# Kernel optimization log

Hardware: AMD Instinct MI355X
Metric: run time of the kernel (lower is better)

The kernel has to match this reference:

```python
import jax, jax.numpy as jnp
import numpy as np

NB = 256  # images are quantized to 256 intensity levels (uint8 pipeline)


def _histograms(q):
    # q: int32 (BC, N) values in [0, NB)
    BC, N = q.shape
    idx = (q + jnp.arange(BC, dtype=jnp.int32)[:, None] * NB).reshape(-1)
    ones = jnp.ones((BC * N,), dtype=jnp.int32)
    return jax.ops.segment_sum(ones, idx, num_segments=BC * NB).reshape(BC, NB)


def _match_lut(counts_s, counts_r):
    # Fixed-shape emulation of the per-channel np.unique/cumsum/np.interp loop.
    occ_s = counts_s > 0
    occ_r = counts_r > 0
    first_s = jnp.argmax(occ_s)  # smallest unique source value (dropped, maps to 0)
    first_r = jnp.argmax(occ_r)  # smallest unique reference value (dropped)
    cs = counts_s.at[first_s].set(0)
    cr = counts_r.at[first_r].set(0)
    cums = jnp.cumsum(cs).astype(jnp.float32)
    cumr = jnp.cumsum(cr).astype(jnp.float32)
    s_q = cums / jnp.maximum(cums[-1], 1.0)  # source quantiles at every bin
    r_q = cumr / jnp.maximum(cumr[-1], 1.0)
    # Compact occupied reference bins (excluding the first) to the front so that
    # jnp.interp sees only the quantiles/values that np.unique would produce.
    occ_r2 = occ_r & (jnp.arange(NB) != first_r)
    order = jnp.argsort(jnp.logical_not(occ_r2))  # stable: occupied bins first, ascending
    occ_sorted = occ_r2[order]
    xp = jnp.where(occ_sorted, r_q[order], 2.0)   # pad with x>1 so queries (<=1) never reach pads
    fp = jnp.where(occ_sorted, order.astype(jnp.float32), 0.0)
    lut = jnp.trunc(jnp.interp(s_q, xp, fp))  # trunc == C-style cast into uint8 result buffer
    lut = lut.at[first_s].set(0.0)            # interp_value[0] = 0 in the original
    ok = (jnp.sum(occ_s) > 1) & (jnp.sum(occ_r) > 1)  # 'continue' branch -> zeros
    return jnp.where(ok, lut, 0.0)


def _match_histogram(source, reference):
    # source/reference: float (B,3,H,W) with values at exact 0..255 levels
    B, C, H, W = source.shape
    sq = jnp.clip(jnp.round(source), 0, NB - 1).astype(jnp.int32).reshape(B * C, H * W)
    rq = jnp.clip(jnp.round(reference), 0, NB - 1).astype(jnp.int32).reshape(B * C, H * W)
    lut = jax.vmap(_match_lut)(_histograms(sq), _histograms(rq))  # (BC, NB)
    return jnp.take_along_axis(lut, sq, axis=1).reshape(B, C, H, W)


def reference(input_data, target_data, ref_data, mask_src, mask_tar):
    to_img = lambda x: (x + 1.0) * 0.5 * 255.0  # tensor2image(x) * 255
    inp = to_img(input_data)
    tar = to_img(target_data)
    ref = to_img(ref_data)
    m_src = jnp.broadcast_to(mask_src, inp.shape)
    m_tar = jnp.broadcast_to(mask_tar, tar.shape)
    input_masked = inp * m_src
    target_masked = tar * m_tar
    ref_masked = ref * m_src
    matched = jax.lax.stop_gradient(_match_histogram(ref_masked, target_masked))
    input_match = matched * m_src
    return jnp.mean(jnp.abs(input_masked - input_match))  # L1Loss


def setup_inputs() -> dict:
    key = jax.random.key(0)
    k1, k2, k3, k4, k5 = jax.random.split(key, 5)
    B, H, W = 8, 512, 512

    def img(k):
        # exact multiples of 1/255 in [-1,1] -> integer 0..255 after tensor2image*255
        levels = jax.random.randint(k, (B, 3, H, W), 0, 256).astype(jnp.float32)
        return (levels / 255.0) * 2.0 - 1.0

    def mask(k):
        return (jax.random.uniform(k, (B, 1, H, W)) > 0.3).astype(jnp.float32)

    return {
        "input_data": img(k1),
        "target_data": img(k2),
        "ref_data": img(k3),
        "mask_src": mask(k4),
        "mask_tar": mask(k5),
    }
```

## Files before the change

### kernel.cpp

```cpp
#include <hip/hip_runtime.h>

#define HW    262144
#define HW4   65536
#define BC    24
#define NB    256
#define NTOT  6291456

#define GH    64
#define GL    64
#define TOTL  (BC * GL)

#define WS_HSP_OFF   0
#define WS_HRP_OFF   1572864
#define WS_LUT_OFF   3145728
#define WS_LSUM_OFF  3170304
#define WS_QB_OFF    3176448
#define WS_MB_OFF    9467904

__device__ __forceinline__ int quantize(float x, float m) {
    float v = (x + 1.0f) * 0.5f * 255.0f * m;
    float r = rintf(v);
    r = fminf(fmaxf(r, 0.0f), 255.0f);
    return (int)r;
}

__device__ __forceinline__ int incl_scan256(int v, int t, int* buf4, int* tot) {
    const int lane = t & 63;
    const int wave = t >> 6;
#pragma unroll
    for (int off = 1; off < 64; off <<= 1) {
        int y = __shfl_up(v, off, 64);
        if (lane >= off) v += y;
    }
    __syncthreads();
    if (lane == 63) buf4[wave] = v;
    __syncthreads();
    int add = 0;
#pragma unroll
    for (int w = 0; w < 4; ++w) if (w < wave) add += buf4[w];
    *tot = buf4[0] + buf4[1] + buf4[2] + buf4[3];
    return v + add;
}

__global__ void __launch_bounds__(256)
hist_kernel(const float4* __restrict__ ref4,
            const float4* __restrict__ tar4,
            const float4* __restrict__ ms4,
            const float4* __restrict__ mt4,
            int* __restrict__ hsPart, int* __restrict__ hrPart,
            uchar4* __restrict__ qb, unsigned short* __restrict__ mb) {
    __shared__ int wh[4 * 2 * NB];
    const int t = threadIdx.x;
    const int wave = t >> 6;
    const int lane = t & 63;
#pragma unroll
    for (int j = 0; j < 8; ++j) wh[t + j * 256] = 0;
    __syncthreads();

    const int c = blockIdx.y;
    const int b = c / 3;
    const float4* refc = ref4 + (size_t)c * HW4;
    const float4* tarc = tar4 + (size_t)c * HW4;
    const float4* msb  = ms4 + (size_t)b * HW4;
    const float4* mtb  = mt4 + (size_t)b * HW4;
    uchar4* qbc = qb + (size_t)c * HW4;
    unsigned short* mbc = mb + (size_t)c * (GH * 256);

    const int base = blockIdx.x * 256 + t;

    float4 R[4], T[4], M[4], MT[4];
#pragma unroll
    for (int j = 0; j < 4; ++j) R[j]  = refc[base + j * 16384];
#pragma unroll
    for (int j = 0; j < 4; ++j) M[j]  = msb[base + j * 16384];
#pragma unroll
    for (int j = 0; j < 4; ++j) T[j]  = tarc[base + j * 16384];
#pragma unroll
    for (int j = 0; j < 4; ++j) MT[j] = mtb[base + j * 16384];

    int* whS = &wh[wave * 512];
    int* whR = &wh[wave * 512 + 256];
    int n0s = 0, n0r = 0;
    unsigned mbits = 0u;
#pragma unroll
    for (int j = 0; j < 4; ++j) {
        const float rv[4]  = {R[j].x, R[j].y, R[j].z, R[j].w};
        const float mv[4]  = {M[j].x, M[j].y, M[j].z, M[j].w};
        const float tvv[4] = {T[j].x, T[j].y, T[j].z, T[j].w};
        const float mtv[4] = {MT[j].x, MT[j].y, MT[j].z, MT[j].w};
        unsigned q8[4];
#pragma unroll
        for (int k = 0; k < 4; ++k) {
            const int qs = quantize(rv[k], mv[k]);
            q8[k] = (unsigned)qs;
            if (mv[k] != 0.0f) { atomicAdd(&whS[qs], 1); mbits |= 1u << (j * 4 + k); }
            else n0s++;
            if (mtv[k] != 0.0f) atomicAdd(&whR[quantize(tvv[k], mtv[k])], 1);
            else n0r++;
        }
        uchar4 qq;
        qq.x = (unsigned char)q8[0];
        qq.y = (unsigned char)q8[1];
        qq.z = (unsigned char)q8[2];
        qq.w = (unsigned char)q8[3];
        qbc[base + j * 16384] = qq;
    }
    mbc[base] = (unsigned short)mbits;

#pragma unroll
    for (int off = 32; off > 0; off >>= 1) {
        n0s += __shfl_down(n0s, off);
        n0r += __shfl_down(n0r, off);
    }
    if (lane == 0) {
        if (n0s) atomicAdd(&whS[0], n0s);
        if (n0r) atomicAdd(&whR[0], n0r);
    }
    __syncthreads();

    const int s = wh[t] + wh[512 + t] + wh[1024 + t] + wh[1536 + t];
    const int r = wh[256 + t] + wh[768 + t] + wh[1280 + t] + wh[1792 + t];
    hsPart[(c * GH + blockIdx.x) * NB + t] = s;
    hrPart[(c * GH + blockIdx.x) * NB + t] = r;
}

__global__ void __launch_bounds__(256)
lut_kernel(const int* __restrict__ hsPart,
           const int* __restrict__ hrPart,
           float* __restrict__ lut) {
    const int c = blockIdx.x;
    const int t = threadIdx.x;

    __shared__ int   buf4[4];
    __shared__ float xp[NB];
    __shared__ float fp[NB];
    __shared__ int firstS, firstR, nOccS, nOccR;

    int cs = 0, cr = 0;
#pragma unroll 8
    for (int g = 0; g < GH; ++g) {
        cs += hsPart[(c * GH + g) * NB + t];
        cr += hrPart[(c * GH + g) * NB + t];
    }

    if (t == 0) { firstS = NB; firstR = NB; nOccS = 0; nOccR = 0; }
    __syncthreads();
    if (cs > 0) { atomicMin(&firstS, t); atomicAdd(&nOccS, 1); }
    if (cr > 0) { atomicMin(&firstR, t); atomicAdd(&nOccR, 1); }
    __syncthreads();

    const int csz = (t == firstS) ? 0 : cs;
    const int crz = (t == firstR) ? 0 : cr;

    int totS, totR, dummy;
    const int cumS = incl_scan256(csz, t, buf4, &totS);
    const int cumR = incl_scan256(crz, t, buf4, &totR);
    const int occ2 = (cr > 0 && t != firstR) ? 1 : 0;
    const int rank = incl_scan256(occ2, t, buf4, &dummy) - occ2;

    const float x  = (float)cumS / fmaxf((float)totS, 1.0f);
    const float rq = (float)cumR / fmaxf((float)totR, 1.0f);

    xp[t] = 2.0f;
    fp[t] = 0.0f;
    __syncthreads();
    if (occ2) { xp[rank] = rq; fp[rank] = (float)t; }
    __syncthreads();

    int lo = 0, hi = NB;
    while (lo < hi) {
        int mid = (lo + hi) >> 1;
        if (xp[mid] > x) hi = mid; else lo = mid + 1;
    }
    int i2 = lo;
    i2 = (i2 < 1) ? 1 : ((i2 > NB - 1) ? NB - 1 : i2);
    float dxv = xp[i2] - xp[i2 - 1];
    float f;
    if (dxv == 0.0f) f = fp[i2];
    else f = fp[i2 - 1] + (x - xp[i2 - 1]) / dxv * (fp[i2] - fp[i2 - 1]);
    if (x < xp[0]) f = fp[0];

    float l = truncf(f);
    if (t == firstS) l = 0.0f;
    if (!((nOccS > 1) && (nOccR > 1))) l = 0.0f;

    lut[c * NB + t] = l;
}

__global__ void __launch_bounds__(256)
loss_kernel(const float4* __restrict__ inp4,
            const uchar4* __restrict__ qb,
            const unsigned short* __restrict__ mb,
            const float* __restrict__ lut,
            float* __restrict__ lsum) {
    __shared__ float llut[NB];
    __shared__ float wsum[4];
    const int t = threadIdx.x;
    const int c = blockIdx.y;
    const int g = blockIdx.x;
    const int lane = t & 63;
    const int wave = t >> 6;

    const float4* inpc = inp4 + (size_t)c * HW4;
    const uchar4* qbc  = qb + (size_t)c * HW4;
    const unsigned short* mbc = mb + (size_t)c * (GL * 256);
    const int base = g * 256 + t;

    float4 X[4];
    uchar4 Q[4];
#pragma unroll
    for (int j = 0; j < 4; ++j) X[j] = inpc[base + j * 16384];
#pragma unroll
    for (int j = 0; j < 4; ++j) Q[j] = qbc[base + j * 16384];
    const unsigned mbits = (unsigned)mbc[base];

    llut[t] = lut[c * NB + t];
    __syncthreads();

    float s = 0.0f;
#pragma unroll
    for (int j = 0; j < 4; ++j) {
        const float xv[4] = {X[j].x, X[j].y, X[j].z, X[j].w};
        const unsigned qv[4] = {Q[j].x, Q[j].y, Q[j].z, Q[j].w};
#pragma unroll
        for (int k = 0; k < 4; ++k) {
            const float mf = (float)((mbits >> (j * 4 + k)) & 1u);
            const float im = (xv[k] + 1.0f) * 127.5f;
            s += mf * fabsf(im - llut[qv[k]]);
        }
    }

#pragma unroll
    for (int off = 32; off > 0; off >>= 1) s += __shfl_down(s, off);
    if (lane == 0) wsum[wave] = s;
    __syncthreads();
    if (t == 0)
        lsum[c * GL + g] = wsum[0] + wsum[1] + wsum[2] + wsum[3];
}

__global__ void __launch_bounds__(256)
finalize_kernel(const float* __restrict__ lsum, float* __restrict__ out) {
    const int t = threadIdx.x;
    float s = 0.0f;
#pragma unroll
    for (int i = t; i < TOTL; i += 256) s += lsum[i];
#pragma unroll
    for (int off = 32; off > 0; off >>= 1) s += __shfl_down(s, off);
    __shared__ float wsum[4];
    const int lane = t & 63;
    const int wave = t >> 6;
    if (lane == 0) wsum[wave] = s;
    __syncthreads();
    if (t == 0)
        out[0] = (wsum[0] + wsum[1] + wsum[2] + wsum[3]) / (float)NTOT;
}

extern "C" void kernel_launch(void* const* d_in, const int* in_sizes, int n_in,
                              void* d_out, int out_size, void* d_ws, size_t ws_size,
                              hipStream_t stream) {
    const float* inp  = (const float*)d_in[0];
    const float* tar  = (const float*)d_in[1];
    const float* ref  = (const float*)d_in[2];
    const float* msrc = (const float*)d_in[3];
    const float* mtar = (const float*)d_in[4];

    char* ws = (char*)d_ws;
    int*            hsPart = (int*)(ws + WS_HSP_OFF);
    int*            hrPart = (int*)(ws + WS_HRP_OFF);
    float*          lut    = (float*)(ws + WS_LUT_OFF);
    float*          lsum   = (float*)(ws + WS_LSUM_OFF);
    uchar4*         qb     = (uchar4*)(ws + WS_QB_OFF);
    unsigned short* mb     = (unsigned short*)(ws + WS_MB_OFF);

    hist_kernel<<<dim3(GH, BC), 256, 0, stream>>>(
        (const float4*)ref, (const float4*)tar,
        (const float4*)msrc, (const float4*)mtar,
        hsPart, hrPart, qb, mb);

    lut_kernel<<<BC, 256, 0, stream>>>(hsPart, hrPart, lut);

    loss_kernel<<<dim3(GL, BC), 256, 0, stream>>>(
        (const float4*)inp, qb, mb, lut, lsum);

    finalize_kernel<<<1, 256, 0, stream>>>(lsum, (float*)d_out);
}
```

Measured before the change: 129.0 us.

## Split histogram merge into its own kernel and fuse LUT build into loss

Replaces the 24-block LUT kernel with a merge kernel that sums the partial histograms across 48 blocks, one per channel and histogram. Each loss block then rebuilds the channel LUT itself (scans, binary-search interp) while its input loads are in flight. The intent is to widen parallelism on the serial LUT stage and overlap LUT construction with the loss loads. In exchange, the scan and interp work is repeated in each of the 64 loss blocks per channel, and the loss kernel uses more shared memory and registers.

```diff
diff --git a/kernel.cpp b/kernel.cpp
--- a/kernel.cpp
+++ b/kernel.cpp
@@ -12,10 +12,11 @@
 
 #define WS_HSP_OFF   0
 #define WS_HRP_OFF   1572864
-#define WS_LUT_OFF   3145728
-#define WS_LSUM_OFF  3170304
-#define WS_QB_OFF    3176448
-#define WS_MB_OFF    9467904
+#define WS_HSF_OFF   3145728
+#define WS_HRF_OFF   3170304
+#define WS_LSUM_OFF  3194880
+#define WS_QB_OFF    3201024
+#define WS_MB_OFF    9492480
 
 __device__ __forceinline__ int quantize(float x, float m) {
     float v = (x + 1.0f) * 0.5f * 255.0f * m;
@@ -125,23 +126,53 @@
 }
 
 __global__ void __launch_bounds__(256)
-lut_kernel(const int* __restrict__ hsPart,
-           const int* __restrict__ hrPart,
-           float* __restrict__ lut) {
-    const int c = blockIdx.x;
-    const int t = threadIdx.x;
-
+merge_kernel(const int* __restrict__ hsPart, const int* __restrict__ hrPart,
+             int* __restrict__ histS, int* __restrict__ histR) {
+    const int c = blockIdx.y;
+    const int t = threadIdx.x;
+    const int* __restrict__ src = blockIdx.x ? hrPart : hsPart;
+    int* __restrict__ dst       = blockIdx.x ? histR : histS;
+    int s = 0;
+#pragma unroll 8
+    for (int g = 0; g < GH; ++g) s += src[(c * GH + g) * NB + t];
+    dst[c * NB + t] = s;
+}
+
+__global__ void __launch_bounds__(256)
+loss_kernel(const float4* __restrict__ inp4,
+            const uchar4* __restrict__ qb,
+            const unsigned short* __restrict__ mb,
+            const int* __restrict__ histS,
+            const int* __restrict__ histR,
+            float* __restrict__ lsum) {
     __shared__ int   buf4[4];
     __shared__ float xp[NB];
     __shared__ float fp[NB];
+    __shared__ float llut[NB];
+    __shared__ float wsum[4];
     __shared__ int firstS, firstR, nOccS, nOccR;
 
-    int cs = 0, cr = 0;
-#pragma unroll 8
-    for (int g = 0; g < GH; ++g) {
-        cs += hsPart[(c * GH + g) * NB + t];
-        cr += hrPart[(c * GH + g) * NB + t];
-    }
+    const int t = threadIdx.x;
+    const int c = blockIdx.y;
+    const int g = blockIdx.x;
+    const int lane = t & 63;
+    const int wave = t >> 6;
+
+    const float4* inpc = inp4 + (size_t)c * HW4;
+    const uchar4* qbc  = qb + (size_t)c * HW4;
+    const unsigned short* mbc = mb + (size_t)c * (GL * 256);
+    const int base = g * 256 + t;
+
+    float4 X[4];
+    uchar4 Q[4];
+#pragma unroll
+    for (int j = 0; j < 4; ++j) X[j] = inpc[base + j * 16384];
+#pragma unroll
+    for (int j = 0; j < 4; ++j) Q[j] = qbc[base + j * 16384];
+    const unsigned mbits = (unsigned)mbc[base];
+
+    const int cs = histS[c * NB + t];
+    const int cr = histR[c * NB + t];
 
     if (t == 0) { firstS = NB; firstR = NB; nOccS = 0; nOccR = 0; }
     __syncthreads();
@@ -184,37 +215,7 @@
     if (t == firstS) l = 0.0f;
     if (!((nOccS > 1) && (nOccR > 1))) l = 0.0f;
 
-    lut[c * NB + t] = l;
-}
-
-__global__ void __launch_bounds__(256)
-loss_kernel(const float4* __restrict__ inp4,
-            const uchar4* __restrict__ qb,
-            const unsigned short* __restrict__ mb,
-            const float* __restrict__ lut,
-            float* __restrict__ lsum) {
-    __shared__ float llut[NB];
-    __shared__ float wsum[4];
-    const int t = threadIdx.x;
-    const int c = blockIdx.y;
-    const int g = blockIdx.x;
-    const int lane = t & 63;
-    const int wave = t >> 6;
-
-    const float4* inpc = inp4 + (size_t)c * HW4;
-    const uchar4* qbc  = qb + (size_t)c * HW4;
-    const unsigned short* mbc = mb + (size_t)c * (GL * 256);
-    const int base = g * 256 + t;
-
-    float4 X[4];
-    uchar4 Q[4];
-#pragma unroll
-    for (int j = 0; j < 4; ++j) X[j] = inpc[base + j * 16384];
-#pragma unroll
-    for (int j = 0; j < 4; ++j) Q[j] = qbc[base + j * 16384];
-    const unsigned mbits = (unsigned)mbc[base];
-
-    llut[t] = lut[c * NB + t];
+    llut[t] = l;
     __syncthreads();
 
     float s = 0.0f;
@@ -267,7 +268,8 @@
     char* ws = (char*)d_ws;
     int*            hsPart = (int*)(ws + WS_HSP_OFF);
     int*            hrPart = (int*)(ws + WS_HRP_OFF);
-    float*          lut    = (float*)(ws + WS_LUT_OFF);
+    int*            histS  = (int*)(ws + WS_HSF_OFF);
+    int*            histR  = (int*)(ws + WS_HRF_OFF);
     float*          lsum   = (float*)(ws + WS_LSUM_OFF);
     uchar4*         qb     = (uchar4*)(ws + WS_QB_OFF);
     unsigned short* mb     = (unsigned short*)(ws + WS_MB_OFF);
@@ -277,10 +279,10 @@
         (const float4*)msrc, (const float4*)mtar,
         hsPart, hrPart, qb, mb);
 
-    lut_kernel<<<BC, 256, 0, stream>>>(hsPart, hrPart, lut);
+    merge_kernel<<<dim3(2, BC), 256, 0, stream>>>(hsPart, hrPart, histS, histR);
 
     loss_kernel<<<dim3(GL, BC), 256, 0, stream>>>(
-        (const float4*)inp, qb, mb, lut, lsum);
+        (const float4*)inp, qb, mb, histS, histR, lsum);
 
     finalize_kernel<<<1, 256, 0, stream>>>(lsum, (float*)d_out);
 }
```

Measured after the change: 132.7 us. +2.8%, slower.
